# Kernel optimization log

Hardware: AMD Instinct MI355X
Metric: run time of the kernel (lower is better)

## Reference

```python
import jax, jax.numpy as jnp
import numpy as np

N = 50000      # nodes
E = 800000     # edges
D = 256        # hidden_dim (input node features)
A = 128        # attention_dim = attention_ratio * heads
H = 8          # heads
DK = A // H    # 16


def setup_inputs() -> dict:
    key = jax.random.key(0)
    ks = jax.random.split(key, 6)
    x = jax.random.normal(ks[0], (N, D), dtype=jnp.float32)
    # small weight scale keeps exp(pre) well-conditioned (module uses tiny const init)
    Wq = jax.random.normal(ks[1], (A, D), dtype=jnp.float32) * 0.02
    bq = jnp.full((A,), 0.01, dtype=jnp.float32)
    Wk = jax.random.normal(ks[2], (A, D), dtype=jnp.float32) * 0.02
    bk = jnp.full((A,), 0.01, dtype=jnp.float32)
    edge_index = jax.random.randint(ks[3], (2, E), 0, N, dtype=jnp.int32)
    # d0_index[1] holds the two node indices each duplicated edge score scatters to
    d0_index = jax.random.randint(ks[4], (2, 2 * E), 0, N, dtype=jnp.int32)
    return {"x": x, "Wq": Wq, "bq": bq, "Wk": Wk, "bk": bk,
            "edge_index": edge_index, "d0_index": d0_index}


def reference(x, Wq, bq, Wk, bk, edge_index, d0_index):
    # linear projections -> [N, H, DK]
    q = (x @ Wq.T + bq).reshape(N, H, DK)
    k = (x @ Wk.T + bk).reshape(N, H, DK)
    src, dst = edge_index[0], edge_index[1]
    q_i = q[src]   # [E, H, DK]
    k_j = k[dst]
    q_j = q[dst]
    k_i = k[src]
    # symmetrized scaled-dot attention score per edge/head
    pre = 0.5 * jnp.sum(q_i * k_j + q_j * k_i, axis=-1)  # [E, H]
    pre = jnp.mean(pre, axis=-1)                          # [E]
    diagA1 = jnp.exp(pre)
    # duplicate each edge score: (a, a, b, b, ...) == torch (view(-1,1)*ones(E,2)).view(-1)
    edge_score_per_node = jnp.repeat(diagA1, 2)           # [2E]
    diagA0 = jax.ops.segment_sum(edge_score_per_node, d0_index[1], num_segments=N)
    return diagA0, diagA1
```

## Files before the change

### kernel.cpp

```cpp
#include <hip/hip_runtime.h>
#include <hip/hip_bf16.h>

#define N_NODES 50000
#define N_EDGES 800000
#define DIM 256
#define QKDIM 256

typedef __bf16 bfrag  __attribute__((ext_vector_type(8)));
typedef __bf16 bf4    __attribute__((ext_vector_type(4)));
typedef float  ffrag  __attribute__((ext_vector_type(4)));
typedef float  f2     __attribute__((ext_vector_type(2)));
typedef float  f4v    __attribute__((ext_vector_type(4)));

#define EP_PITCH 272

__global__ __launch_bounds__(256) void prep_kernel(
    const float* __restrict__ Wq, const float* __restrict__ Wk,
    __bf16* __restrict__ Wb, float* __restrict__ out)
{
    const int tid = blockIdx.x * 256 + threadIdx.x;
    const int i = tid * 4;
    const float* s = (i < 32768) ? (Wq + i) : (Wk + (i - 32768));
    const float4 v = *(const float4*)s;
    bf4 o;
    o[0] = (__bf16)v.x; o[1] = (__bf16)v.y; o[2] = (__bf16)v.z; o[3] = (__bf16)v.w;
    *(bf4*)(Wb + i) = o;

    if (i + 4 <= N_NODES)
        *(float4*)(out + i) = make_float4(0.f, 0.f, 0.f, 0.f);
}

__global__ __launch_bounds__(256) void proj_mfma(
    const float* __restrict__ x,
    const __bf16* __restrict__ Wb,
    const float* __restrict__ bq, const float* __restrict__ bk,
    unsigned char* __restrict__ qk8)
{
    __shared__ __bf16 As[64 * 256];

    const int tid  = threadIdx.x;
    const int wv   = tid >> 6;
    const int lane = tid & 63;
    const int m    = lane & 15;
    const int q    = lane >> 4;
    const int mbase = blockIdx.x * 64;

    {
        const int srow = tid >> 2;
        const int c4   = tid & 3;
        int grow = mbase + srow;
        grow = grow < N_NODES ? grow : N_NODES - 1;
        const float* xp = x + (size_t)grow * DIM;
        const int mt_ = srow >> 4, m_ = srow & 15;
        #pragma unroll
        for (int i = 0; i < 16; ++i) {
            const int k = c4 * 4 + 16 * i;
            const f4v v = __builtin_nontemporal_load((const f4v*)(xp + k));
            bf4 o;
            o[0] = (__bf16)v[0]; o[1] = (__bf16)v[1];
            o[2] = (__bf16)v[2]; o[3] = (__bf16)v[3];
            const int seg = (k >> 5) * 4 + mt_;
            const int ln  = ((k >> 3) & 3) * 16 + m_;
            *(bf4*)(As + seg * 512 + ln * 8 + (k & 7)) = o;
        }
    }
    __syncthreads();

    ffrag acc[4][4] = {};

    #pragma unroll
    for (int h = 0; h < 2; ++h) {
        bfrag b[4][4];
        #pragma unroll
        for (int sp = 0; sp < 4; ++sp)
            #pragma unroll
            for (int nt = 0; nt < 4; ++nt) {
                const int col = wv * 64 + nt * 16 + m;
                b[sp][nt] = *(const bfrag*)(Wb + (size_t)col * DIM
                                            + 32 * (4 * h + sp) + 8 * q);
            }
        #pragma unroll
        for (int sp = 0; sp < 4; ++sp) {
            bfrag a[4];
            #pragma unroll
            for (int mt = 0; mt < 4; ++mt)
                a[mt] = *(const bfrag*)(As + ((4 * h + sp) * 4 + mt) * 512 + lane * 8);
            #pragma unroll
            for (int mt = 0; mt < 4; ++mt)
                #pragma unroll
                for (int nt = 0; nt < 4; ++nt)
                    acc[mt][nt] = __builtin_amdgcn_mfma_f32_16x16x32_bf16(
                                      a[mt], b[sp][nt], acc[mt][nt], 0, 0, 0);
        }
    }

    __syncthreads();
    unsigned char* ep = (unsigned char*)As;
    #pragma unroll
    for (int nt = 0; nt < 4; ++nt) {
        const int col  = wv * 64 + nt * 16 + m;
        const float bias = (col < 128) ? bq[col] : bk[col - 128];
        #pragma unroll
        for (int mt = 0; mt < 4; ++mt) {
            #pragma unroll
            for (int r = 0; r < 4; ++r) {
                const int rl = mt * 16 + q * 4 + r;
                const float v = acc[mt][nt][r] + bias;
                const int pk = __builtin_amdgcn_cvt_pk_fp8_f32(v, v, 0, false);
                ep[rl * EP_PITCH + col] = (unsigned char)(pk & 0xFF);
            }
        }
    }
    __syncthreads();
    {
        const int rl = tid >> 2;
        const int ch = tid & 3;
        const int grow = mbase + rl;
        if (grow < N_NODES) {
            const uint4* s4 = (const uint4*)(ep + rl * EP_PITCH + ch * 64);
            const uint4 t0 = s4[0], t1 = s4[1], t2 = s4[2], t3 = s4[3];
            uint4* g = (uint4*)(qk8 + (size_t)grow * QKDIM + ch * 64);
            g[0] = t0; g[1] = t1; g[2] = t2; g[3] = t3;
        }
    }
}

__global__ __launch_bounds__(256) void edge_kernel(
    const unsigned char* __restrict__ qk8,
    const int* __restrict__ edge_index,
    const int* __restrict__ d0,
    float* __restrict__ out)
{
    const int wave = (blockIdx.x * blockDim.x + threadIdx.x) >> 6;
    const int lane = threadIdx.x & 63;
    const int g = lane >> 2;
    const int j = lane & 3;
    const int e = wave * 16 + g;

    const int src = __builtin_nontemporal_load(edge_index + e);
    const int dst = __builtin_nontemporal_load(edge_index + N_EDGES + e);

    const uint4* rs = (const uint4*)(qk8 + (size_t)src * QKDIM + 64 * j);
    const uint4* rd = (const uint4*)(qk8 + (size_t)dst * QKDIM + 64 * ((j + 2) & 3));

    uint4 a[4], b[4];
    #pragma unroll
    for (int i = 0; i < 4; ++i) { a[i] = rs[i]; b[i] = rd[i]; }

    f2 acc = {0.f, 0.f};
    #pragma unroll
    for (int i = 0; i < 4; ++i) {
        const unsigned int* ua = (const unsigned int*)&a[i];
        const unsigned int* ub = (const unsigned int*)&b[i];
        #pragma unroll
        for (int t = 0; t < 4; ++t) {
            const f2 x0 = __builtin_amdgcn_cvt_pk_f32_fp8(ua[t], false);
            const f2 y0 = __builtin_amdgcn_cvt_pk_f32_fp8(ub[t], false);
            const f2 x1 = __builtin_amdgcn_cvt_pk_f32_fp8(ua[t], true);
            const f2 y1 = __builtin_amdgcn_cvt_pk_f32_fp8(ub[t], true);
            acc += x0 * y0;
            acc += x1 * y1;
        }
    }
    float p = acc[0] + acc[1];

    p += __shfl_xor(p, 1, 64);
    p += __shfl_xor(p, 2, 64);

    if (j < 2) {
        const float val = __expf(p * 0.0625f);
        const int target = __builtin_nontemporal_load(d0 + 2 * e + j);
        if (j == 0) __builtin_nontemporal_store(val, out + N_NODES + e);
        atomicAdd(&out[target], val);
    }
}

extern "C" void kernel_launch(void* const* d_in, const int* in_sizes, int n_in,
                              void* d_out, int out_size, void* d_ws, size_t ws_size,
                              hipStream_t stream) {
    const float* x  = (const float*)d_in[0];
    const float* Wq = (const float*)d_in[1];
    const float* bq = (const float*)d_in[2];
    const float* Wk = (const float*)d_in[3];
    const float* bk = (const float*)d_in[4];
    const int* edge_index = (const int*)d_in[5];
    const int* d0 = (const int*)d_in[6] + 2 * N_EDGES;
    float* out = (float*)d_out;

    unsigned char* qk8 = (unsigned char*)d_ws;
    __bf16* Wb = (__bf16*)((char*)d_ws + (size_t)N_NODES * QKDIM);

    prep_kernel<<<64, 256, 0, stream>>>(Wq, Wk, Wb, out);
    proj_mfma<<<(N_NODES + 63) / 64, 256, 0, stream>>>(x, Wb, bq, bk, qk8);

    edge_kernel<<<N_EDGES / 64, 256, 0, stream>>>(qk8, edge_index, d0, out);
}
```

Baseline: 223.3 us.

## Privatize scatter-add into eight accumulator copies and reduce afterwards

Edge blocks now spread their atomic adds over eight private copies of the node accumulator, chosen by block index, to reduce contention on the atomics. A new reduce kernel sums the copies into the output. The prep kernel grows to zero the copies, and the path falls back to direct atomics when the workspace is too small. The cost is an extra kernel launch, about 1.6 MB more memory traffic, and a larger memset.

```diff
diff --git a/kernel.cpp b/kernel.cpp
--- a/kernel.cpp
+++ b/kernel.cpp
@@ -5,6 +5,7 @@
 #define N_EDGES 800000
 #define DIM 256
 #define QKDIM 256
+#define N_COPIES 8
 
 typedef __bf16 bfrag  __attribute__((ext_vector_type(8)));
 typedef __bf16 bf4    __attribute__((ext_vector_type(4)));
@@ -16,18 +17,25 @@
 
 __global__ __launch_bounds__(256) void prep_kernel(
     const float* __restrict__ Wq, const float* __restrict__ Wk,
-    __bf16* __restrict__ Wb, float* __restrict__ out)
+    __bf16* __restrict__ Wb, float* __restrict__ out,
+    float* __restrict__ priv, int flag)
 {
     const int tid = blockIdx.x * 256 + threadIdx.x;
     const int i = tid * 4;
-    const float* s = (i < 32768) ? (Wq + i) : (Wk + (i - 32768));
-    const float4 v = *(const float4*)s;
-    bf4 o;
-    o[0] = (__bf16)v.x; o[1] = (__bf16)v.y; o[2] = (__bf16)v.z; o[3] = (__bf16)v.w;
-    *(bf4*)(Wb + i) = o;
-
-    if (i + 4 <= N_NODES)
-        *(float4*)(out + i) = make_float4(0.f, 0.f, 0.f, 0.f);
+    if (i < 65536) {
+        const float* s = (i < 32768) ? (Wq + i) : (Wk + (i - 32768));
+        const float4 v = *(const float4*)s;
+        bf4 o;
+        o[0] = (__bf16)v.x; o[1] = (__bf16)v.y; o[2] = (__bf16)v.z; o[3] = (__bf16)v.w;
+        *(bf4*)(Wb + i) = o;
+    }
+    if (flag) {
+        if (tid < (N_COPIES * N_NODES) / 4)
+            ((float4*)priv)[tid] = make_float4(0.f, 0.f, 0.f, 0.f);
+    } else {
+        if (i + 4 <= N_NODES)
+            *(float4*)(out + i) = make_float4(0.f, 0.f, 0.f, 0.f);
+    }
 }
 
 __global__ __launch_bounds__(256) void proj_mfma(
@@ -129,13 +137,16 @@
     const unsigned char* __restrict__ qk8,
     const int* __restrict__ edge_index,
     const int* __restrict__ d0,
-    float* __restrict__ out)
+    float* __restrict__ out,
+    float* __restrict__ accum, int copymask)
 {
     const int wave = (blockIdx.x * blockDim.x + threadIdx.x) >> 6;
     const int lane = threadIdx.x & 63;
     const int g = lane >> 2;
     const int j = lane & 3;
     const int e = wave * 16 + g;
+
+    float* myacc = accum + (size_t)(blockIdx.x & copymask) * N_NODES;
 
     const int src = __builtin_nontemporal_load(edge_index + e);
     const int dst = __builtin_nontemporal_load(edge_index + N_EDGES + e);
@@ -171,7 +182,20 @@
         const float val = __expf(p * 0.0625f);
         const int target = __builtin_nontemporal_load(d0 + 2 * e + j);
         if (j == 0) __builtin_nontemporal_store(val, out + N_NODES + e);
-        atomicAdd(&out[target], val);
+        atomicAdd(&myacc[target], val);
+    }
+}
+
+__global__ __launch_bounds__(256) void reduce_kernel(
+    const float* __restrict__ priv, float* __restrict__ out)
+{
+    const int idx = (blockIdx.x * 256 + threadIdx.x) * 4;
+    if (idx < N_NODES) {
+        f4v s = __builtin_nontemporal_load((const f4v*)(priv + idx));
+        #pragma unroll
+        for (int c = 1; c < N_COPIES; ++c)
+            s += __builtin_nontemporal_load((const f4v*)(priv + (size_t)c * N_NODES + idx));
+        *(f4v*)(out + idx) = s;
     }
 }
 
@@ -189,9 +213,19 @@
 
     unsigned char* qk8 = (unsigned char*)d_ws;
     __bf16* Wb = (__bf16*)((char*)d_ws + (size_t)N_NODES * QKDIM);
-
-    prep_kernel<<<64, 256, 0, stream>>>(Wq, Wk, Wb, out);
+    float* priv = (float*)((char*)d_ws + (size_t)N_NODES * QKDIM + 131072);
+
+    const size_t needed = (size_t)N_NODES * QKDIM + 131072
+                        + (size_t)N_COPIES * N_NODES * sizeof(float);
+    const int use_priv = (ws_size >= needed) ? 1 : 0;
+    float* accum = use_priv ? priv : out;
+    const int copymask = use_priv ? (N_COPIES - 1) : 0;
+
+    prep_kernel<<<391, 256, 0, stream>>>(Wq, Wk, Wb, out, priv, use_priv);
     proj_mfma<<<(N_NODES + 63) / 64, 256, 0, stream>>>(x, Wb, bq, bk, qk8);
 
-    edge_kernel<<<N_EDGES / 64, 256, 0, stream>>>(qk8, edge_index, d0, out);
-}
+    edge_kernel<<<N_EDGES / 64, 256, 0, stream>>>(qk8, edge_index, d0, out,
+                                                  accum, copymask);
+    if (use_priv)
+        reduce_kernel<<<(N_NODES / 4 + 255) / 256, 256, 0, stream>>>(priv, out);
+}
```

After: 216.4 us. 1.03x faster.

## Replace global atomic scatter with binned two-phase segment sum

Applied to the files above, without the earlier changes.

Global atomicAdd for the segment sum is replaced by binning: the prep kernel groups the 1.6M target indices into 391 bins of 128 nodes, writing packed (local node, edge) records. A new scatter kernel then reduces each bin with shared-memory atomics and writes the node sums directly, so the output no longer needs zeroing. The goal is to remove contended global atomics, at the cost of an extra memset, an extra kernel, record traffic, and a gather of edge scores. It relies on a fixed per-bin capacity of 8192, which could overflow for skewed inputs.

```diff
diff --git a/kernel.cpp b/kernel.cpp
--- a/kernel.cpp
+++ b/kernel.cpp
@@ -5,6 +5,10 @@
 #define N_EDGES 800000
 #define DIM 256
 #define QKDIM 256
+#define NB_T  391
+#define CAP   8192
+#define ITEMS (2 * N_EDGES)
+#define IPB   4096
 
 typedef __bf16 bfrag  __attribute__((ext_vector_type(8)));
 typedef __bf16 bf4    __attribute__((ext_vector_type(4)));
@@ -14,20 +18,56 @@
 
 #define EP_PITCH 272
 
-__global__ __launch_bounds__(256) void prep_kernel(
+__global__ __launch_bounds__(256) void prep_bin(
     const float* __restrict__ Wq, const float* __restrict__ Wk,
-    __bf16* __restrict__ Wb, float* __restrict__ out)
-{
-    const int tid = blockIdx.x * 256 + threadIdx.x;
-    const int i = tid * 4;
-    const float* s = (i < 32768) ? (Wq + i) : (Wk + (i - 32768));
-    const float4 v = *(const float4*)s;
-    bf4 o;
-    o[0] = (__bf16)v.x; o[1] = (__bf16)v.y; o[2] = (__bf16)v.z; o[3] = (__bf16)v.w;
-    *(bf4*)(Wb + i) = o;
-
-    if (i + 4 <= N_NODES)
-        *(float4*)(out + i) = make_float4(0.f, 0.f, 0.f, 0.f);
+    __bf16* __restrict__ Wb,
+    const int* __restrict__ d0, unsigned int* __restrict__ rec,
+    int* __restrict__ cur)
+{
+    __shared__ int lcnt[NB_T];
+    __shared__ int lbase[NB_T];
+    const int tid = threadIdx.x;
+    const int gtid = blockIdx.x * 256 + tid;
+
+    const int i4 = gtid * 4;
+    if (i4 < 65536) {
+        const float* s = (i4 < 32768) ? (Wq + i4) : (Wk + (i4 - 32768));
+        const float4 v = *(const float4*)s;
+        bf4 o;
+        o[0] = (__bf16)v.x; o[1] = (__bf16)v.y; o[2] = (__bf16)v.z; o[3] = (__bf16)v.w;
+        *(bf4*)(Wb + i4) = o;
+    }
+
+    for (int b = tid; b < NB_T; b += 256) lcnt[b] = 0;
+    __syncthreads();
+    const int base = blockIdx.x * IPB;
+    int tg[16];
+    #pragma unroll
+    for (int r = 0; r < 16; ++r) {
+        const int i = base + r * 256 + tid;
+        tg[r] = (i < ITEMS) ? d0[i] : -1;
+        if (tg[r] >= 0) atomicAdd(&lcnt[tg[r] >> 7], 1);
+    }
+    __syncthreads();
+
+    for (int b = tid; b < NB_T; b += 256) {
+        const int c = lcnt[b];
+        lbase[b] = c ? atomicAdd(&cur[b], c) : 0;
+    }
+    __syncthreads();
+    for (int b = tid; b < NB_T; b += 256) lcnt[b] = 0;
+    __syncthreads();
+
+    #pragma unroll
+    for (int r = 0; r < 16; ++r) {
+        if (tg[r] >= 0) {
+            const int i = base + r * 256 + tid;
+            const int b = tg[r] >> 7;
+            const int off = atomicAdd(&lcnt[b], 1);
+            rec[(size_t)b * CAP + lbase[b] + off] =
+                ((unsigned int)(tg[r] & 127) << 20) | (unsigned int)(i >> 1);
+        }
+    }
 }
 
 __global__ __launch_bounds__(256) void proj_mfma(
@@ -125,10 +165,9 @@
     }
 }
 
-__global__ __launch_bounds__(256) void edge_kernel(
+__global__ __launch_bounds__(256) void edge_compute(
     const unsigned char* __restrict__ qk8,
     const int* __restrict__ edge_index,
-    const int* __restrict__ d0,
     float* __restrict__ out)
 {
     const int wave = (blockIdx.x * blockDim.x + threadIdx.x) >> 6;
@@ -167,11 +206,32 @@
     p += __shfl_xor(p, 1, 64);
     p += __shfl_xor(p, 2, 64);
 
-    if (j < 2) {
-        const float val = __expf(p * 0.0625f);
-        const int target = __builtin_nontemporal_load(d0 + 2 * e + j);
-        if (j == 0) __builtin_nontemporal_store(val, out + N_NODES + e);
-        atomicAdd(&out[target], val);
+    if (j == 0)
+        out[N_NODES + e] = __expf(p * 0.0625f);
+}
+
+__global__ __launch_bounds__(1024) void phase_scatter(
+    const unsigned int* __restrict__ rec, const int* __restrict__ cur,
+    float* __restrict__ out)
+{
+    __shared__ float acc[128];
+    const int b = blockIdx.x;
+    const int tid = threadIdx.x;
+    if (tid < 128) acc[tid] = 0.f;
+    __syncthreads();
+
+    const int cnt = cur[b];
+    const unsigned int* rb = rec + (size_t)b * CAP;
+    for (int i = tid; i < cnt; i += 1024) {
+        const unsigned int r = rb[i];
+        const float v = out[N_NODES + (r & 0xFFFFF)];
+        atomicAdd(&acc[r >> 20], v);
+    }
+    __syncthreads();
+
+    if (tid < 128) {
+        const int n = b * 128 + tid;
+        if (n < N_NODES) out[n] = acc[tid];
     }
 }
 
@@ -187,11 +247,15 @@
     const int* d0 = (const int*)d_in[6] + 2 * N_EDGES;
     float* out = (float*)d_out;
 
-    unsigned char* qk8 = (unsigned char*)d_ws;
-    __bf16* Wb = (__bf16*)((char*)d_ws + (size_t)N_NODES * QKDIM);
-
-    prep_kernel<<<64, 256, 0, stream>>>(Wq, Wk, Wb, out);
+    char* w = (char*)d_ws;
+    unsigned char* qk8 = (unsigned char*)w;  w += (size_t)N_NODES * QKDIM;
+    __bf16* Wb = (__bf16*)w;                 w += 131072;
+    unsigned int* rec = (unsigned int*)w;    w += (size_t)NB_T * CAP * 4;
+    int* cur = (int*)w;                      w += 2048;
+
+    hipMemsetAsync(cur, 0, NB_T * sizeof(int), stream);
+    prep_bin<<<NB_T, 256, 0, stream>>>(Wq, Wk, Wb, d0, rec, cur);
     proj_mfma<<<(N_NODES + 63) / 64, 256, 0, stream>>>(x, Wb, bq, bk, qk8);
-
-    edge_kernel<<<N_EDGES / 64, 256, 0, stream>>>(qk8, edge_index, d0, out);
-}
+    edge_compute<<<N_EDGES / 64, 256, 0, stream>>>(qk8, edge_index, out);
+    phase_scatter<<<NB_T, 1024, 0, stream>>>(rec, cur, out);
+}
```

New measurement: 207.5 us. 1.08x faster.
